# Kernel optimization log

Hardware: AMD Instinct MI355X
Metric: run time of the kernel (lower is better)

The kernel has to match this reference:

```python
import jax, jax.numpy as jnp
import numpy as np

D = 1024; H = 16; HD = 64; L = 8; V = 2048; FF = 4096; WIN = 256
THETA = 10000.0; EPS = 1e-5; LN_EPS = 1e-5; MAXCYC = 16
NM = 16; NR = 72; NT = 12; ME = 64; RE = 64; TE = 32; TPE = 16; DE = 16
B = 2; S = 1024


def _rotate_half(x):
    # torch: stack((-x[...,1::2], x[...,0::2]), -1).flatten(-2)
    x1 = x[..., ::2]
    x2 = x[..., 1::2]
    return jnp.stack((-x2, x1), axis=-1).reshape(x.shape)


def _rmsnorm(x, w):
    return w * (x * jax.lax.rsqrt(jnp.mean(x * x, axis=-1, keepdims=True) + EPS))


def _layernorm(x, g, b):
    mu = jnp.mean(x, axis=-1, keepdims=True)
    var = jnp.mean((x - mu) ** 2, axis=-1, keepdims=True)
    return (x - mu) * jax.lax.rsqrt(var + LN_EPS) * g + b


def setup_inputs() -> dict:
    key = jax.random.key(0)
    ks = iter(jax.random.split(key, 64))
    w = lambda shape: jax.random.normal(next(ks), shape, jnp.float32) * 0.02
    inp = {
        'tokens': jax.random.randint(next(ks), (B, S), 0, V),
        'mood': jax.random.randint(next(ks), (B,), 0, NM),
        'raga': jax.random.randint(next(ks), (B,), 0, NR),
        'taal': jax.random.randint(next(ks), (B,), 0, NT),
        'tempo': jax.random.uniform(next(ks), (B,), jnp.float32),
        'duration': jax.random.uniform(next(ks), (B,), jnp.float32),
        'taal_cycle_len': 8,
        'tok_emb': w((V, D)),
        'mood_emb': w((NM, ME)), 'raga_emb': w((NR, RE)), 'taal_emb': w((NT, TE)),
        'tempo_w': w((TPE, 1)), 'tempo_b': jnp.zeros((TPE,), jnp.float32),
        'dur_w': w((DE, 1)), 'dur_b': jnp.zeros((DE,), jnp.float32),
        'proj_w': w((D, ME + RE + TE + TPE + DE)), 'proj_b': jnp.zeros((D,), jnp.float32),
        'ln_g': jnp.ones((D,), jnp.float32), 'ln_b': jnp.zeros((D,), jnp.float32),
        'cycle_emb': w((MAXCYC, D)), 'strength_emb': w((4, D)),
        'l_anorm': jnp.ones((L, D), jnp.float32), 'l_fnorm': jnp.ones((L, D), jnp.float32),
        'l_q': w((L, D, D)), 'l_k': w((L, D, D)), 'l_v': w((L, D, D)), 'l_o': w((L, D, D)),
        'l_w1': w((L, FF, D)), 'l_w2': w((L, D, FF)), 'l_w3': w((L, FF, D)),
        'final_norm': jnp.ones((D,), jnp.float32),
        'head_w': w((V, D)),
    }
    return inp


def reference(tokens, mood, raga, taal, tempo, duration, taal_cycle_len,
              tok_emb, mood_emb, raga_emb, taal_emb, tempo_w, tempo_b, dur_w, dur_b,
              proj_w, proj_b, ln_g, ln_b, cycle_emb, strength_emb,
              l_anorm, l_fnorm, l_q, l_k, l_v, l_o, l_w1, l_w2, l_w3,
              final_norm, head_w):
    bsz, seq_len = tokens.shape
    # --- ConditioningModule ---
    tp = tempo[:, None] * tempo_w[:, 0][None, :] + tempo_b      # Linear(1, TPE)
    dp = duration[:, None] * dur_w[:, 0][None, :] + dur_b       # Linear(1, DE)
    cond = jnp.concatenate([mood_emb[mood], raga_emb[raga], taal_emb[taal], tp, dp], axis=-1)
    cond = jax.nn.gelu(cond @ proj_w.T + proj_b, approximate=False)
    cond = _layernorm(cond, ln_g, ln_b)                          # [B, D]
    # --- TaalPositionEncoder (taal_cycle_len is static python int) ---
    cyc = min(int(taal_cycle_len), MAXCYC)
    pos_emb = cycle_emb[jnp.arange(seq_len) % cyc]
    strengths = jnp.full((seq_len,), 3, jnp.int32).at[::int(taal_cycle_len)].set(0)
    taal_pos = pos_emb + strength_emb[strengths]                 # [S, D]
    # --- input embedding ---
    x = tok_emb[tokens] + cond[:, None, :] + taal_pos[None]      # [B, S, D]
    # --- RoPE tables (scaling=1.0) ---
    inv_freq = 1.0 / (THETA ** (jnp.arange(0, HD, 2, jnp.float32) / HD))
    freqs = jnp.outer(jnp.arange(seq_len, dtype=jnp.float32), inv_freq)
    emb = jnp.concatenate([freqs, freqs], axis=-1)               # [S, HD]
    cos = jnp.cos(emb)[None, None]
    sin = jnp.sin(emb)[None, None]
    # --- causal sliding-window mask bias ---
    idx = jnp.arange(seq_len)
    allow = (idx[:, None] >= idx[None, :]) & (idx[:, None] - idx[None, :] < WIN)
    bias = jnp.where(allow, 0.0, -jnp.inf).astype(x.dtype)       # [S, S]
    scale = 1.0 / np.sqrt(HD)

    def block(x, p):
        an, fn, qw, kw, vw, ow, w1, w2, w3 = p
        h = _rmsnorm(x, an)
        q = (h @ qw.T).reshape(bsz, seq_len, H, HD).transpose(0, 2, 1, 3)
        k = (h @ kw.T).reshape(bsz, seq_len, H, HD).transpose(0, 2, 1, 3)
        v = (h @ vw.T).reshape(bsz, seq_len, H, HD).transpose(0, 2, 1, 3)
        q = q * cos + _rotate_half(q) * sin
        k = k * cos + _rotate_half(k) * sin
        scores = jnp.einsum('bhqd,bhkd->bhqk', q, k) * scale + bias
        attn = jax.nn.softmax(scores, axis=-1)
        y = jnp.einsum('bhqk,bhkd->bhqd', attn, v)
        y = y.transpose(0, 2, 1, 3).reshape(bsz, seq_len, D)
        x = x + y @ ow.T
        h2 = _rmsnorm(x, fn)
        x = x + (jax.nn.silu(h2 @ w1.T) * (h2 @ w3.T)) @ w2.T
        return x, None

    x, _ = jax.lax.scan(block, x, (l_anorm, l_fnorm, l_q, l_k, l_v, l_o, l_w1, l_w2, l_w3))
    x = _rmsnorm(x, final_norm)
    return x @ head_w.T                                          # [B, S, V] logits
```

## Files before the change

### kernel.cpp

```cpp
#include <hip/hip_runtime.h>
#include <math.h>

#define D_ 1024
#define H_ 16
#define HD_ 64
#define L_ 8
#define V_ 2048
#define FF_ 4096
#define WIN_ 256
#define B_ 2
#define S_ 1024
#define MAXCYC_ 16

typedef __attribute__((ext_vector_type(4))) float f32x4;
typedef __attribute__((ext_vector_type(8))) short s16x8;

__device__ __forceinline__ unsigned short f2bf(float f) {
  union { float f; unsigned int u; } v; v.f = f;
  unsigned int r = v.u + 0x7FFFu + ((v.u >> 16) & 1u);
  return (unsigned short)(r >> 16);
}

__device__ __forceinline__ float wave_sum(float v) {
  #pragma unroll
  for (int m = 1; m < 64; m <<= 1) v += __shfl_xor(v, m, 64);
  return v;
}

__device__ __forceinline__ void gload16(const unsigned short* g, unsigned short* lds) {
  __builtin_amdgcn_global_load_lds(
      (const __attribute__((address_space(1))) void*)g,
      (__attribute__((address_space(3))) void*)lds,
      16, 0, 0);
}

__global__ __launch_bounds__(256) void cvt_kernel(
    const float* __restrict__ src, unsigned short* __restrict__ dst, int n8)
{
  int i = blockIdx.x*256 + threadIdx.x;
  if (i >= n8) return;
  const float4* s = (const float4*)src + (size_t)i*2;
  float4 a = s[0], b = s[1];
  ushort4 lo, hi;
  lo.x = f2bf(a.x); lo.y = f2bf(a.y); lo.z = f2bf(a.z); lo.w = f2bf(a.w);
  hi.x = f2bf(b.x); hi.y = f2bf(b.y); hi.z = f2bf(b.z); hi.w = f2bf(b.w);
  *(ushort4*)(dst + (size_t)i*8)     = lo;
  *(ushort4*)(dst + (size_t)i*8 + 4) = hi;
}

__global__ __launch_bounds__(256) void cond_kernel(
    const int* mood, const int* raga, const int* taal,
    const float* tempo, const float* duration,
    const float* mood_emb, const float* raga_emb, const float* taal_emb,
    const float* tempo_w, const float* tempo_b, const float* dur_w, const float* dur_b,
    const float* proj_w, const float* proj_b, const float* ln_g, const float* ln_b,
    float* cond)
{
  int b = blockIdx.x;
  int t = threadIdx.x;
  __shared__ float feat[192];
  __shared__ float red[4];
  if (t < 64)        feat[t] = mood_emb[mood[b]*64 + t];
  else if (t < 128)  feat[t] = raga_emb[raga[b]*64 + (t-64)];
  else if (t < 160)  feat[t] = taal_emb[taal[b]*32 + (t-128)];
  else if (t < 176)  feat[t] = tempo[b]*tempo_w[t-160] + tempo_b[t-160];
  else if (t < 192)  feat[t] = duration[b]*dur_w[t-176] + dur_b[t-176];
  __syncthreads();
  float g[4];
  #pragma unroll
  for (int r = 0; r < 4; ++r) {
    int j = t + 256*r;
    const float* w = proj_w + (size_t)j*192;
    float acc = proj_b[j];
    for (int f = 0; f < 192; ++f) acc += feat[f]*w[f];
    g[r] = 0.5f * acc * (1.0f + erff(acc * 0.7071067811865475f));
  }
  int lane = t & 63, wv = t >> 6;
  float s1 = g[0]+g[1]+g[2]+g[3];
  s1 = wave_sum(s1);
  if (lane == 0) red[wv] = s1;
  __syncthreads();
  float mu = (red[0]+red[1]+red[2]+red[3]) * (1.0f/1024.0f);
  __syncthreads();
  float vs = 0.f;
  #pragma unroll
  for (int r = 0; r < 4; ++r) { float d = g[r]-mu; vs += d*d; }
  vs = wave_sum(vs);
  if (lane == 0) red[wv] = vs;
  __syncthreads();
  float var = (red[0]+red[1]+red[2]+red[3]) * (1.0f/1024.0f);
  float is = rsqrtf(var + 1e-5f);
  #pragma unroll
  for (int r = 0; r < 4; ++r) {
    int j = t + 256*r;
    cond[(size_t)b*D_ + j] = (g[r]-mu)*is*ln_g[j] + ln_b[j];
  }
}

__global__ __launch_bounds__(256) void embed_kernel(
    const int* tokens, const float* tok_emb, const float* cond,
    const float* cycle_emb, const float* strength_emb, const int* tcl_p, float* x)
{
  int row = blockIdx.x;
  int b = row >> 10, s = row & 1023;
  int tcl = tcl_p[0];
  int cyc = tcl < MAXCYC_ ? tcl : MAXCYC_;
  int pr  = s % cyc;
  int str = (s % tcl == 0) ? 0 : 3;
  int tok = tokens[row];
  int d = threadIdx.x * 4;
  float4 a = *(const float4*)&tok_emb[(size_t)tok*D_ + d];
  float4 c = *(const float4*)&cond[(size_t)b*D_ + d];
  float4 p = *(const float4*)&cycle_emb[(size_t)pr*D_ + d];
  float4 e = *(const float4*)&strength_emb[(size_t)str*D_ + d];
  float4 o; o.x=a.x+c.x+p.x+e.x; o.y=a.y+c.y+p.y+e.y; o.z=a.z+c.z+p.z+e.z; o.w=a.w+c.w+p.w+e.w;
  *(float4*)&x[(size_t)row*D_ + d] = o;
}

__global__ __launch_bounds__(256) void rmsnorm_kernel(
    const float* x, const float* w, unsigned short* out)
{
  int row = blockIdx.x;
  int t = threadIdx.x;
  __shared__ float red[4];
  const float* xr = x + (size_t)row*D_;
  float4 v = *(const float4*)&xr[t*4];
  float ss = v.x*v.x + v.y*v.y + v.z*v.z + v.w*v.w;
  ss = wave_sum(ss);
  int lane = t & 63, wv = t >> 6;
  if (lane == 0) red[wv] = ss;
  __syncthreads();
  float total = red[0]+red[1]+red[2]+red[3];
  float scale = rsqrtf(total * (1.0f/1024.0f) + 1e-5f);
  float4 wv4 = *(const float4*)&w[t*4];
  ushort4 o;
  o.x = f2bf(wv4.x * v.x * scale);
  o.y = f2bf(wv4.y * v.y * scale);
  o.z = f2bf(wv4.z * v.z * scale);
  o.w = f2bf(wv4.w * v.w * scale);
  *(ushort4*)&out[(size_t)row*D_ + t*4] = o;
}

__global__ __launch_bounds__(256) void rope_table_kernel(float* costab, float* sintab)
{
  int i = blockIdx.x*256 + threadIdx.x;
  int s = i >> 6, d = i & 63;
  float inv = powf(10000.0f, -(float)(d & 31) * (1.0f/32.0f));
  float ang = (float)s * inv;
  float sn, cs;
  sincosf(ang, &sn, &cs);
  costab[i] = cs; sintab[i] = sn;
}

__global__ __launch_bounds__(256) void attn_mfma(
    const unsigned short* __restrict__ q, const unsigned short* __restrict__ k,
    const unsigned short* __restrict__ v, unsigned short* __restrict__ y)
{
  __shared__ unsigned short Ks[64*64];
  __shared__ unsigned short VsT[64*72];
  __shared__ unsigned short Ps[4*16*72];

  int qb0 = blockIdx.x * 64;
  int h = blockIdx.y, b = blockIdx.z;
  int t = threadIdx.x, lane = t & 63, wv = t >> 6;
  int c = lane & 15, q4 = lane >> 4;
  unsigned short* Pw = &Ps[wv*16*72];

  s16x8 aq[2];
  {
    const unsigned short* qp =
        q + ((size_t)(b*S_ + qb0 + wv*16 + c)*D_ + h*HD_ + q4*8);
    aq[0] = *(const s16x8*)qp;
    aq[1] = *(const s16x8*)(qp + 32);
  }

  f32x4 o[4];
  #pragma unroll
  for (int j = 0; j < 4; ++j) o[j] = (f32x4){0.f,0.f,0.f,0.f};
  float m[4] = {-1e30f,-1e30f,-1e30f,-1e30f};
  float l[4] = {0.f,0.f,0.f,0.f};

  int skey = t >> 2;
  int scol = (t & 3) * 16;
  int kt0 = qb0 - 256; if (kt0 < 0) kt0 = 0;

  for (int kt = kt0; kt <= qb0; kt += 64) {
    __syncthreads();
    {
      const unsigned short* kp = k + ((size_t)(b*S_ + kt + skey)*D_ + h*HD_ + scol);
      s16x8 k0 = *(const s16x8*)kp;
      s16x8 k1 = *(const s16x8*)(kp + 8);
      int ch0 = scol >> 3;
      *(s16x8*)((char*)Ks + skey*128 + ((ch0 ^ (skey & 7)) << 4)) = k0;
      *(s16x8*)((char*)Ks + skey*128 + (((ch0+1) ^ (skey & 7)) << 4)) = k1;
      const unsigned short* vp = v + ((size_t)(b*S_ + kt + skey)*D_ + h*HD_ + scol);
      s16x8 v0 = *(const s16x8*)vp;
      s16x8 v1 = *(const s16x8*)(vp + 8);
      #pragma unroll
      for (int i = 0; i < 8; ++i) {
        VsT[(scol + i)*72 + skey]     = (unsigned short)v0[i];
        VsT[(scol + 8 + i)*72 + skey] = (unsigned short)v1[i];
      }
    }
    __syncthreads();

    f32x4 sa[4];
    #pragma unroll
    for (int j = 0; j < 4; ++j) sa[j] = (f32x4){0.f,0.f,0.f,0.f};
    #pragma unroll
    for (int ks = 0; ks < 2; ++ks)
      #pragma unroll
      for (int j = 0; j < 4; ++j) {
        int key = j*16 + c;
        s16x8 bk = *(const s16x8*)((const char*)Ks + key*128 +
                                   (((q4 + ks*4) ^ (key & 7)) << 4));
        sa[j] = __builtin_amdgcn_mfma_f32_16x16x32_bf16(aq[ks], bk, sa[j], 0, 0, 0);
      }

    float sv[4][4];
    #pragma unroll
    for (int j = 0; j < 4; ++j) {
      int kg = kt + j*16 + c;
      #pragma unroll
      for (int reg = 0; reg < 4; ++reg) {
        int qg = qb0 + wv*16 + q4*4 + reg;
        bool ok = (qg >= kg) && (qg - kg < WIN_);
        sv[j][reg] = ok ? sa[j][reg]*0.125f : -3e38f;
      }
    }
    #pragma unroll
    for (int reg = 0; reg < 4; ++reg) {
      float mx = fmaxf(fmaxf(sv[0][reg], sv[1][reg]), fmaxf(sv[2][reg], sv[3][reg]));
      #pragma unroll
      for (int msk = 1; msk < 16; msk <<= 1)
        mx = fmaxf(mx, __shfl_xor(mx, msk, 64));
      float nm = fmaxf(m[reg], mx);
      float f = __expf(m[reg] - nm);
      m[reg] = nm;
      l[reg] *= f;
      o[0][reg] *= f; o[1][reg] *= f; o[2][reg] *= f; o[3][reg] *= f;
      float ps = 0.f;
      #pragma unroll
      for (int j = 0; j < 4; ++j) {
        float p = __expf(sv[j][reg] - nm);
        ps += p;
        Pw[(q4*4 + reg)*72 + j*16 + c] = f2bf(p);
      }
      l[reg] += ps;
    }

    #pragma unroll
    for (int ks = 0; ks < 2; ++ks) {
      s16x8 pa = *(const s16x8*)((const char*)Pw + c*144 + (q4 + ks*4)*16);
      #pragma unroll
      for (int j = 0; j < 4; ++j) {
        s16x8 bv = *(const s16x8*)((const char*)VsT + (j*16 + c)*144 + (q4 + ks*4)*16);
        o[j] = __builtin_amdgcn_mfma_f32_16x16x32_bf16(pa, bv, o[j], 0, 0, 0);
      }
    }
  }

  float inv[4];
  #pragma unroll
  for (int reg = 0; reg < 4; ++reg) {
    float ll = l[reg];
    #pragma unroll
    for (int msk = 1; msk < 16; msk <<= 1) ll += __shfl_xor(ll, msk, 64);
    inv[reg] = 1.0f / ll;
  }
  #pragma unroll
  for (int j = 0; j < 4; ++j)
    #pragma unroll
    for (int reg = 0; reg < 4; ++reg)
      Pw[(q4*4 + reg)*72 + j*16 + c] = f2bf(o[j][reg] * inv[reg]);
  int lr = lane >> 2, cc = (lane & 3)*16;
  s16x8 y0 = *(const s16x8*)((const char*)Pw + lr*144 + cc*2);
  s16x8 y1 = *(const s16x8*)((const char*)Pw + lr*144 + cc*2 + 16);
  unsigned short* yp = y + ((size_t)(b*S_ + qb0 + wv*16 + lr)*D_ + h*HD_ + cc);
  *(s16x8*)yp = y0;
  *(s16x8*)(yp + 8) = y1;
}

__global__ __launch_bounds__(256, 2) void gemm_w13(
    const unsigned short* __restrict__ A,
    const unsigned short* __restrict__ W1, const unsigned short* __restrict__ W3,
    unsigned short* __restrict__ T, int K, int lda, int ldw)
{
  __shared__ unsigned short sA[2][128*32];
  __shared__ unsigned short sW1[2][128*32];
  __shared__ unsigned short sW3[2][128*32];
  int tid = threadIdx.x, lane = tid & 63, wave = tid >> 6;
  int wr = (wave >> 1)*64, wc = (wave & 1)*64;
  size_t bm = (size_t)blockIdx.x*128, bn = (size_t)blockIdx.y*128;
  int fr = lane & 15, fk = (lane >> 4)*8, fq = (lane >> 4)*4;
  int rseg = lane >> 2, chunk = (lane & 3)*8;

  f32x4 a1[4][4], a3[4][4];
  #pragma unroll
  for (int i = 0; i < 4; ++i)
    #pragma unroll
    for (int j = 0; j < 4; ++j) {
      a1[i][j] = (f32x4){0.f,0.f,0.f,0.f};
      a3[i][j] = (f32x4){0.f,0.f,0.f,0.f};
    }

  auto stage = [&](int buf, int kt) {
    #pragma unroll
    for (int p = 0; p < 2; ++p) {
      int seg = wave*2 + p;
      int row = seg*16 + rseg;
      gload16(A  + (bm + row)*(size_t)lda + kt + chunk, &sA[buf][seg*512]);
      gload16(W1 + (bn + row)*(size_t)ldw + kt + chunk, &sW1[buf][seg*512]);
      gload16(W3 + (bn + row)*(size_t)ldw + kt + chunk, &sW3[buf][seg*512]);
    }
  };

  stage(0, 0);
  __syncthreads();
  int nt = K >> 5;
  for (int t = 0; t < nt; ++t) {
    int cur = t & 1;
    if (t + 1 < nt) stage(cur ^ 1, (t+1)*32);
    s16x8 af[4], b1[4], b3[4];
    #pragma unroll
    for (int i = 0; i < 4; ++i) {
      af[i] = *(const s16x8*)&sA[cur][(wr + i*16 + fr)*32 + fk];
      b1[i] = *(const s16x8*)&sW1[cur][(wc + i*16 + fr)*32 + fk];
      b3[i] = *(const s16x8*)&sW3[cur][(wc + i*16 + fr)*32 + fk];
    }
    #pragma unroll
    for (int i = 0; i < 4; ++i)
      #pragma unroll
      for (int j = 0; j < 4; ++j) {
        a1[i][j] = __builtin_amdgcn_mfma_f32_16x16x32_bf16(af[i], b1[j], a1[i][j], 0, 0, 0);
        a3[i][j] = __builtin_amdgcn_mfma_f32_16x16x32_bf16(af[i], b3[j], a3[i][j], 0, 0, 0);
      }
    __syncthreads();
  }

  #pragma unroll
  for (int i = 0; i < 4; ++i)
    #pragma unroll
    for (int j = 0; j < 4; ++j) {
      size_t row0 = bm + wr + i*16 + fq;
      size_t col  = bn + wc + j*16 + fr;
      #pragma unroll
      for (int qi = 0; qi < 4; ++qi) {
        float u = a1[i][j][qi];
        float g = a3[i][j][qi];
        float su = u / (1.0f + __expf(-u));
        T[(row0 + qi)*(size_t)FF_ + col] = f2bf(su * g);
      }
    }
}

template<int EPI>
__device__ __forceinline__ void gemm64_core(
    const unsigned short* __restrict__ A, const unsigned short* __restrict__ W,
    float* __restrict__ Cf, unsigned short* __restrict__ Cb,
    int K, int lda, int ldw, int ldc,
    const float* __restrict__ costab, const float* __restrict__ sintab)
{
  __shared__ unsigned short sA[2][128*32];
  __shared__ unsigned short sW[2][64*32];
  int tid = threadIdx.x, lane = tid & 63, wave = tid >> 6;
  int wr = (wave >> 1)*64, wc = (wave & 1)*32;
  size_t bm = (size_t)blockIdx.x*128, bn = (size_t)blockIdx.y*64;
  int fr = lane & 15, fk = (lane >> 4)*8, fq = (lane >> 4)*4;
  int rseg = lane >> 2, chunk = (lane & 3)*8;

  f32x4 acc[4][2];
  #pragma unroll
  for (int i = 0; i < 4; ++i) {
    acc[i][0] = (f32x4){0.f,0.f,0.f,0.f};
    acc[i][1] = (f32x4){0.f,0.f,0.f,0.f};
  }

  auto stage = [&](int buf, int kt) {
    #pragma unroll
    for (int p = 0; p < 2; ++p) {
      int seg = wave*2 + p;
      int row = seg*16 + rseg;
      gload16(A + (bm + row)*(size_t)lda + kt + chunk, &sA[buf][seg*512]);
    }
    int row = wave*16 + rseg;
    gload16(W + (bn + row)*(size_t)ldw + kt + chunk, &sW[buf][wave*512]);
  };

  stage(0, 0);
  __syncthreads();
  int nt = K >> 5;
  for (int t = 0; t < nt; ++t) {
    int cur = t & 1;
    if (t + 1 < nt) stage(cur ^ 1, (t+1)*32);
    s16x8 af[4], bw[2];
    #pragma unroll
    for (int i = 0; i < 4; ++i)
      af[i] = *(const s16x8*)&sA[cur][(wr + i*16 + fr)*32 + fk];
    #pragma unroll
    for (int j = 0; j < 2; ++j)
      bw[j] = *(const s16x8*)&sW[cur][(wc + j*16 + fr)*32 + fk];
    #pragma unroll
    for (int i = 0; i < 4; ++i)
      #pragma unroll
      for (int j = 0; j < 2; ++j)
        acc[i][j] = __builtin_amdgcn_mfma_f32_16x16x32_bf16(af[i], bw[j], acc[i][j], 0, 0, 0);
    __syncthreads();
  }

  #pragma unroll
  for (int i = 0; i < 4; ++i)
    #pragma unroll
    for (int j = 0; j < 2; ++j) {
      size_t row0 = bm + wr + i*16 + fq;
      size_t col  = bn + wc + j*16 + fr;
      #pragma unroll
      for (int qi = 0; qi < 4; ++qi) {
        float val = acc[i][j][qi];
        size_t idx = (row0 + qi)*(size_t)ldc + col;
        if (EPI == 3) {
          float pv = __shfl_xor(val, 1, 64);
          int srow = (int)((row0 + qi) & 1023);
          int d = (int)(col & 63);
          float cs = costab[srow*64 + d];
          float sn = sintab[srow*64 + d];
          Cb[idx] = f2bf(val*cs + ((d & 1) ? pv : -pv)*sn);
        } else if (EPI == 4) {
          Cb[idx] = f2bf(val);
        } else if (EPI == 1) {
          Cf[idx] += val;
        } else {
          Cf[idx] = val;
        }
      }
    }
}

template<int EPI>
__global__ __launch_bounds__(256) void gemm64(
    const unsigned short* __restrict__ A, const unsigned short* __restrict__ W,
    float* __restrict__ Cf, int K, int lda, int ldw, int ldc)
{
  gemm64_core<EPI>(A, W, Cf, nullptr, K, lda, ldw, ldc, nullptr, nullptr);
}

__global__ __launch_bounds__(256) void gemm_qkv64(
    const unsigned short* __restrict__ A,
    const unsigned short* __restrict__ Wq, const unsigned short* __restrict__ Wk,
    const unsigned short* __restrict__ Wv,
    unsigned short* __restrict__ Cq, unsigned short* __restrict__ Ck,
    unsigned short* __restrict__ Cv,
    const float* __restrict__ costab, const float* __restrict__ sintab)
{
  if (blockIdx.z == 0)
    gemm64_core<3>(A, Wq, nullptr, Cq, D_, D_, D_, D_, costab, sintab);
  else if (blockIdx.z == 1)
    gemm64_core<3>(A, Wk, nullptr, Ck, D_, D_, D_, D_, costab, sintab);
  else
    gemm64_core<4>(A, Wv, nullptr, Cv, D_, D_, D_, D_, nullptr, nullptr);
}

extern "C" void kernel_launch(void* const* d_in, const int* in_sizes, int n_in,
                              void* d_out, int out_size, void* d_ws, size_t ws_size,
                              hipStream_t stream)
{
  const int*   tokens    = (const int*)d_in[0];
  const int*   mood      = (const int*)d_in[1];
  const int*   raga      = (const int*)d_in[2];
  const int*   taal      = (const int*)d_in[3];
  const float* tempo     = (const float*)d_in[4];
  const float* duration  = (const float*)d_in[5];
  const int*   tcl       = (const int*)d_in[6];
  const float* tok_emb   = (const float*)d_in[7];
  const float* mood_emb  = (const float*)d_in[8];
  const float* raga_emb  = (const float*)d_in[9];
  const float* taal_emb  = (const float*)d_in[10];
  const float* tempo_w   = (const float*)d_in[11];
  const float* tempo_b   = (const float*)d_in[12];
  const float* dur_w     = (const float*)d_in[13];
  const float* dur_b     = (const float*)d_in[14];
  const float* proj_w    = (const float*)d_in[15];
  const float* proj_b    = (const float*)d_in[16];
  const float* ln_g      = (const float*)d_in[17];
  const float* ln_b      = (const float*)d_in[18];
  const float* cycle_emb = (const float*)d_in[19];
  const float* strength_e= (const float*)d_in[20];
  const float* l_anorm   = (const float*)d_in[21];
  const float* l_fnorm   = (const float*)d_in[22];
  const float* l_q       = (const float*)d_in[23];
  const float* l_k       = (const float*)d_in[24];
  const float* l_v       = (const float*)d_in[25];
  const float* l_o       = (const float*)d_in[26];
  const float* l_w1      = (const float*)d_in[27];
  const float* l_w2      = (const float*)d_in[28];
  const float* l_w3      = (const float*)d_in[29];
  const float* final_norm= (const float*)d_in[30];
  const float* head_w    = (const float*)d_in[31];

  size_t off = 0;
  char* wsb = (char*)d_ws;
  auto alloc = [&](size_t bytes) -> char* {
    char* p = wsb + off;
    off += (bytes + 255) & ~(size_t)255;
    return p;
  };
  float*          condb  = (float*)alloc((size_t)B_*D_*4);
  float*          costab = (float*)alloc((size_t)S_*HD_*4);
  float*          sintab = (float*)alloc((size_t)S_*HD_*4);
  float*          x      = (float*)alloc((size_t)B_*S_*D_*4);
  unsigned short* hbuf   = (unsigned short*)alloc((size_t)B_*S_*D_*2);
  unsigned short* qb     = (unsigned short*)alloc((size_t)B_*S_*D_*2);
  unsigned short* kb     = (unsigned short*)alloc((size_t)B_*S_*D_*2);
  unsigned short* vb     = (unsigned short*)alloc((size_t)B_*S_*D_*2);
  unsigned short* yb     = (unsigned short*)alloc((size_t)B_*S_*D_*2);
  unsigned short* tb     = (unsigned short*)alloc((size_t)B_*S_*FF_*2);

  const size_t N_QKVO = (size_t)L_*D_*D_;
  const size_t N_FF   = (size_t)L_*FF_*D_;
  const size_t N_HEAD = (size_t)V_*D_;
  unsigned short* wbf = (unsigned short*)alloc((4*N_QKVO + 3*N_FF + N_HEAD)*2);
  unsigned short* bq = wbf;
  unsigned short* bk = wbf + N_QKVO;
  unsigned short* bv = wbf + 2*N_QKVO;
  unsigned short* bo = wbf + 3*N_QKVO;
  unsigned short* b1 = wbf + 4*N_QKVO;
  unsigned short* b2 = wbf + 4*N_QKVO + N_FF;
  unsigned short* b3 = wbf + 4*N_QKVO + 2*N_FF;
  unsigned short* bh = wbf + 4*N_QKVO + 3*N_FF;

  rope_table_kernel<<<(S_*HD_)/256, 256, 0, stream>>>(costab, sintab);
  cond_kernel<<<B_, 256, 0, stream>>>(mood, raga, taal, tempo, duration,
      mood_emb, raga_emb, taal_emb, tempo_w, tempo_b, dur_w, dur_b,
      proj_w, proj_b, ln_g, ln_b, condb);
  embed_kernel<<<B_*S_, 256, 0, stream>>>(tokens, tok_emb, condb, cycle_emb,
      strength_e, tcl, x);

  cvt_kernel<<<(int)(N_QKVO/8/256), 256, 0, stream>>>(l_q,  bq, (int)(N_QKVO/8));
  cvt_kernel<<<(int)(N_QKVO/8/256), 256, 0, stream>>>(l_k,  bk, (int)(N_QKVO/8));
  cvt_kernel<<<(int)(N_QKVO/8/256), 256, 0, stream>>>(l_v,  bv, (int)(N_QKVO/8));
  cvt_kernel<<<(int)(N_QKVO/8/256), 256, 0, stream>>>(l_o,  bo, (int)(N_QKVO/8));
  cvt_kernel<<<(int)(N_FF/8/256),   256, 0, stream>>>(l_w1, b1, (int)(N_FF/8));
  cvt_kernel<<<(int)(N_FF/8/256),   256, 0, stream>>>(l_w2, b2, (int)(N_FF/8));
  cvt_kernel<<<(int)(N_FF/8/256),   256, 0, stream>>>(l_w3, b3, (int)(N_FF/8));
  cvt_kernel<<<(int)(N_HEAD/8/256), 256, 0, stream>>>(head_w, bh, (int)(N_HEAD/8));

  const int rows = B_*S_;
  for (int l = 0; l < L_; ++l) {
    size_t dd = (size_t)l*D_*D_;
    size_t fd = (size_t)l*FF_*D_;
    rmsnorm_kernel<<<rows, 256, 0, stream>>>(x, l_anorm + (size_t)l*D_, hbuf);
    gemm_qkv64<<<dim3(rows/128, D_/64, 3), 256, 0, stream>>>(
        hbuf, bq + dd, bk + dd, bv + dd, qb, kb, vb, costab, sintab);
    attn_mfma<<<dim3(S_/64, H_, B_), 256, 0, stream>>>(qb, kb, vb, yb);
    gemm64<1><<<dim3(rows/128, D_/64), 256, 0, stream>>>(
        yb, bo + dd, x, D_, D_, D_, D_);
    rmsnorm_kernel<<<rows, 256, 0, stream>>>(x, l_fnorm + (size_t)l*D_, hbuf);
    gemm_w13<<<dim3(rows/128, FF_/128), 256, 0, stream>>>(
        hbuf, b1 + fd, b3 + fd, tb, D_, D_, D_);
    gemm64<1><<<dim3(rows/128, D_/64), 256, 0, stream>>>(
        tb, b2 + fd, x, FF_, FF_, FF_, D_);
  }
  rmsnorm_kernel<<<rows, 256, 0, stream>>>(x, final_norm, hbuf);
  gemm64<0><<<dim3(rows/128, V_/64), 256, 0, stream>>>(
      hbuf, bh, (float*)d_out, D_, D_, D_, V_);
}
```

Before: 1.898 ms.

## Split-K the O/W2 projections, fuse residual add into RMSNorm, swizzle LDS tiles

Result: faster. 1.782 ms (-6.1%).

```diff
diff --git a/kernel.cpp b/kernel.cpp
--- a/kernel.cpp
+++ b/kernel.cpp
@@ -141,6 +141,37 @@
   *(ushort4*)&out[(size_t)row*D_ + t*4] = o;
 }
 
+__global__ __launch_bounds__(256) void resid_rmsnorm_kernel(
+    float* __restrict__ x, const float* __restrict__ part, int nparts,
+    const float* __restrict__ w, unsigned short* __restrict__ out)
+{
+  int row = blockIdx.x;
+  int t = threadIdx.x;
+  __shared__ float red[4];
+  size_t base = (size_t)row*D_ + t*4;
+  const size_t pstride = (size_t)B_*S_*D_;
+  float4 v = *(const float4*)&x[base];
+  for (int p = 0; p < nparts; ++p) {
+    float4 a = *(const float4*)&part[p*pstride + base];
+    v.x += a.x; v.y += a.y; v.z += a.z; v.w += a.w;
+  }
+  *(float4*)&x[base] = v;
+  float ss = v.x*v.x + v.y*v.y + v.z*v.z + v.w*v.w;
+  ss = wave_sum(ss);
+  int lane = t & 63, wv = t >> 6;
+  if (lane == 0) red[wv] = ss;
+  __syncthreads();
+  float total = red[0]+red[1]+red[2]+red[3];
+  float scale = rsqrtf(total * (1.0f/1024.0f) + 1e-5f);
+  float4 wv4 = *(const float4*)&w[t*4];
+  ushort4 o;
+  o.x = f2bf(wv4.x * v.x * scale);
+  o.y = f2bf(wv4.y * v.y * scale);
+  o.z = f2bf(wv4.z * v.z * scale);
+  o.w = f2bf(wv4.w * v.w * scale);
+  *(ushort4*)&out[(size_t)row*D_ + t*4] = o;
+}
+
 __global__ __launch_bounds__(256) void rope_table_kernel(float* costab, float* sintab)
 {
   int i = blockIdx.x*256 + threadIdx.x;
@@ -292,8 +323,9 @@
   int tid = threadIdx.x, lane = tid & 63, wave = tid >> 6;
   int wr = (wave >> 1)*64, wc = (wave & 1)*64;
   size_t bm = (size_t)blockIdx.x*128, bn = (size_t)blockIdx.y*128;
-  int fr = lane & 15, fk = (lane >> 4)*8, fq = (lane >> 4)*4;
-  int rseg = lane >> 2, chunk = (lane & 3)*8;
+  int fr = lane & 15, q4 = lane >> 4, fq = q4*4;
+  int lrow = lane >> 2;
+  int gcol = ((lane & 3) ^ (lrow & 3)) * 8;
 
   f32x4 a1[4][4], a3[4][4];
   #pragma unroll
@@ -308,10 +340,10 @@
     #pragma unroll
     for (int p = 0; p < 2; ++p) {
       int seg = wave*2 + p;
-      int row = seg*16 + rseg;
-      gload16(A  + (bm + row)*(size_t)lda + kt + chunk, &sA[buf][seg*512]);
-      gload16(W1 + (bn + row)*(size_t)ldw + kt + chunk, &sW1[buf][seg*512]);
-      gload16(W3 + (bn + row)*(size_t)ldw + kt + chunk, &sW3[buf][seg*512]);
+      size_t row = (size_t)(seg*16 + lrow);
+      gload16(A  + (bm + row)*(size_t)lda + kt + gcol, &sA[buf][seg*512]);
+      gload16(W1 + (bn + row)*(size_t)ldw + kt + gcol, &sW1[buf][seg*512]);
+      gload16(W3 + (bn + row)*(size_t)ldw + kt + gcol, &sW3[buf][seg*512]);
     }
   };
 
@@ -324,9 +356,10 @@
     s16x8 af[4], b1[4], b3[4];
     #pragma unroll
     for (int i = 0; i < 4; ++i) {
-      af[i] = *(const s16x8*)&sA[cur][(wr + i*16 + fr)*32 + fk];
-      b1[i] = *(const s16x8*)&sW1[cur][(wc + i*16 + fr)*32 + fk];
-      b3[i] = *(const s16x8*)&sW3[cur][(wc + i*16 + fr)*32 + fk];
+      int ra = wr + i*16 + fr, rb = wc + i*16 + fr;
+      af[i] = *(const s16x8*)((const char*)&sA[cur][0]  + ra*64 + ((q4 ^ (ra & 3)) << 4));
+      b1[i] = *(const s16x8*)((const char*)&sW1[cur][0] + rb*64 + ((q4 ^ (rb & 3)) << 4));
+      b3[i] = *(const s16x8*)((const char*)&sW3[cur][0] + rb*64 + ((q4 ^ (rb & 3)) << 4));
     }
     #pragma unroll
     for (int i = 0; i < 4; ++i)
@@ -358,16 +391,17 @@
 __device__ __forceinline__ void gemm64_core(
     const unsigned short* __restrict__ A, const unsigned short* __restrict__ W,
     float* __restrict__ Cf, unsigned short* __restrict__ Cb,
-    int K, int lda, int ldw, int ldc,
+    int kbase, int Kslice, int lda, int ldw, int ldc,
     const float* __restrict__ costab, const float* __restrict__ sintab)
 {
-  __shared__ unsigned short sA[2][128*32];
-  __shared__ unsigned short sW[2][64*32];
+  __shared__ unsigned short sA[2][128*64];
+  __shared__ unsigned short sW[2][64*64];
   int tid = threadIdx.x, lane = tid & 63, wave = tid >> 6;
   int wr = (wave >> 1)*64, wc = (wave & 1)*32;
   size_t bm = (size_t)blockIdx.x*128, bn = (size_t)blockIdx.y*64;
-  int fr = lane & 15, fk = (lane >> 4)*8, fq = (lane >> 4)*4;
-  int rseg = lane >> 2, chunk = (lane & 3)*8;
+  int fr = lane & 15, q4 = lane >> 4, fq = q4*4;
+  int lrow = lane >> 3;
+  int gcol = ((lane & 7) ^ lrow) * 8;
 
   f32x4 acc[4][2];
   #pragma unroll
@@ -378,33 +412,44 @@
 
   auto stage = [&](int buf, int kt) {
     #pragma unroll
+    for (int p = 0; p < 4; ++p) {
+      int seg = wave*4 + p;
+      gload16(A + (bm + seg*8 + lrow)*(size_t)lda + kt + gcol, &sA[buf][seg*512]);
+    }
+    #pragma unroll
     for (int p = 0; p < 2; ++p) {
       int seg = wave*2 + p;
-      int row = seg*16 + rseg;
-      gload16(A + (bm + row)*(size_t)lda + kt + chunk, &sA[buf][seg*512]);
-    }
-    int row = wave*16 + rseg;
-    gload16(W + (bn + row)*(size_t)ldw + kt + chunk, &sW[buf][wave*512]);
+      gload16(W + (bn + seg*8 + lrow)*(size_t)ldw + kt + gcol, &sW[buf][seg*512]);
+    }
   };
 
-  stage(0, 0);
-  __syncthreads();
-  int nt = K >> 5;
+  stage(0, kbase);
+  __syncthreads();
+  int nt = Kslice >> 6;
   for (int t = 0; t < nt; ++t) {
     int cur = t & 1;
-    if (t + 1 < nt) stage(cur ^ 1, (t+1)*32);
-    s16x8 af[4], bw[2];
-    #pragma unroll
-    for (int i = 0; i < 4; ++i)
-      af[i] = *(const s16x8*)&sA[cur][(wr + i*16 + fr)*32 + fk];
-    #pragma unroll
-    for (int j = 0; j < 2; ++j)
-      bw[j] = *(const s16x8*)&sW[cur][(wc + j*16 + fr)*32 + fk];
-    #pragma unroll
-    for (int i = 0; i < 4; ++i)
-      #pragma unroll
-      for (int j = 0; j < 2; ++j)
-        acc[i][j] = __builtin_amdgcn_mfma_f32_16x16x32_bf16(af[i], bw[j], acc[i][j], 0, 0, 0);
+    if (t + 1 < nt) stage(cur ^ 1, kbase + (t+1)*64);
+    #pragma unroll
+    for (int ks = 0; ks < 2; ++ks) {
+      s16x8 af[4], bw[2];
+      #pragma unroll
+      for (int i = 0; i < 4; ++i) {
+        int r = wr + i*16 + fr;
+        af[i] = *(const s16x8*)((const char*)&sA[cur][0] + r*128 +
+                                ((((ks<<2) + q4) ^ (r & 7)) << 4));
+      }
+      #pragma unroll
+      for (int j = 0; j < 2; ++j) {
+        int r = wc + j*16 + fr;
+        bw[j] = *(const s16x8*)((const char*)&sW[cur][0] + r*128 +
+                                ((((ks<<2) + q4) ^ (r & 7)) << 4));
+      }
+      #pragma unroll
+      for (int i = 0; i < 4; ++i)
+        #pragma unroll
+        for (int j = 0; j < 2; ++j)
+          acc[i][j] = __builtin_amdgcn_mfma_f32_16x16x32_bf16(af[i], bw[j], acc[i][j], 0, 0, 0);
+    }
     __syncthreads();
   }
 
@@ -427,8 +472,6 @@
           Cb[idx] = f2bf(val*cs + ((d & 1) ? pv : -pv)*sn);
         } else if (EPI == 4) {
           Cb[idx] = f2bf(val);
-        } else if (EPI == 1) {
-          Cf[idx] += val;
         } else {
           Cf[idx] = val;
         }
@@ -437,14 +480,23 @@
 }
 
 template<int EPI>
-__global__ __launch_bounds__(256) void gemm64(
+__global__ __launch_bounds__(256, 3) void gemm64(
     const unsigned short* __restrict__ A, const unsigned short* __restrict__ W,
     float* __restrict__ Cf, int K, int lda, int ldw, int ldc)
 {
-  gemm64_core<EPI>(A, W, Cf, nullptr, K, lda, ldw, ldc, nullptr, nullptr);
-}
-
-__global__ __launch_bounds__(256) void gemm_qkv64(
+  gemm64_core<EPI>(A, W, Cf, nullptr, 0, K, lda, ldw, ldc, nullptr, nullptr);
+}
+
+__global__ __launch_bounds__(256, 3) void gemm64_ksplit(
+    const unsigned short* __restrict__ A, const unsigned short* __restrict__ W,
+    float* __restrict__ P, int Kslice, int lda, int ldw, int ldc)
+{
+  float* out = P + (size_t)blockIdx.z * (size_t)B_ * S_ * ldc;
+  gemm64_core<0>(A, W, out, nullptr, blockIdx.z*Kslice, Kslice, lda, ldw, ldc,
+                 nullptr, nullptr);
+}
+
+__global__ __launch_bounds__(256, 3) void gemm_qkv64(
     const unsigned short* __restrict__ A,
     const unsigned short* __restrict__ Wq, const unsigned short* __restrict__ Wk,
     const unsigned short* __restrict__ Wv,
@@ -453,11 +505,11 @@
     const float* __restrict__ costab, const float* __restrict__ sintab)
 {
   if (blockIdx.z == 0)
-    gemm64_core<3>(A, Wq, nullptr, Cq, D_, D_, D_, D_, costab, sintab);
+    gemm64_core<3>(A, Wq, nullptr, Cq, 0, D_, D_, D_, D_, costab, sintab);
   else if (blockIdx.z == 1)
-    gemm64_core<3>(A, Wk, nullptr, Ck, D_, D_, D_, D_, costab, sintab);
+    gemm64_core<3>(A, Wk, nullptr, Ck, 0, D_, D_, D_, D_, costab, sintab);
   else
-    gemm64_core<4>(A, Wv, nullptr, Cv, D_, D_, D_, D_, nullptr, nullptr);
+    gemm64_core<4>(A, Wv, nullptr, Cv, 0, D_, D_, D_, D_, nullptr, nullptr);
 }
 
 extern "C" void kernel_launch(void* const* d_in, const int* in_sizes, int n_in,
@@ -514,6 +566,7 @@
   unsigned short* vb     = (unsigned short*)alloc((size_t)B_*S_*D_*2);
   unsigned short* yb     = (unsigned short*)alloc((size_t)B_*S_*D_*2);
   unsigned short* tb     = (unsigned short*)alloc((size_t)B_*S_*FF_*2);
+  float*          pbuf   = (float*)alloc((size_t)4*B_*S_*D_*4);
 
   const size_t N_QKVO = (size_t)L_*D_*D_;
   const size_t N_FF   = (size_t)L_*FF_*D_;
@@ -545,22 +598,24 @@
   cvt_kernel<<<(int)(N_HEAD/8/256), 256, 0, stream>>>(head_w, bh, (int)(N_HEAD/8));
 
   const int rows = B_*S_;
+  rmsnorm_kernel<<<rows, 256, 0, stream>>>(x, l_anorm, hbuf);
   for (int l = 0; l < L_; ++l) {
     size_t dd = (size_t)l*D_*D_;
     size_t fd = (size_t)l*FF_*D_;
-    rmsnorm_kernel<<<rows, 256, 0, stream>>>(x, l_anorm + (size_t)l*D_, hbuf);
     gemm_qkv64<<<dim3(rows/128, D_/64, 3), 256, 0, stream>>>(
         hbuf, bq + dd, bk + dd, bv + dd, qb, kb, vb, costab, sintab);
     attn_mfma<<<dim3(S_/64, H_, B_), 256, 0, stream>>>(qb, kb, vb, yb);
-    gemm64<1><<<dim3(rows/128, D_/64), 256, 0, stream>>>(
-        yb, bo + dd, x, D_, D_, D_, D_);
-    rmsnorm_kernel<<<rows, 256, 0, stream>>>(x, l_fnorm + (size_t)l*D_, hbuf);
+    gemm64_ksplit<<<dim3(rows/128, D_/64, 2), 256, 0, stream>>>(
+        yb, bo + dd, pbuf, 512, D_, D_, D_);
+    resid_rmsnorm_kernel<<<rows, 256, 0, stream>>>(
+        x, pbuf, 2, l_fnorm + (size_t)l*D_, hbuf);
     gemm_w13<<<dim3(rows/128, FF_/128), 256, 0, stream>>>(
         hbuf, b1 + fd, b3 + fd, tb, D_, D_, D_);
-    gemm64<1><<<dim3(rows/128, D_/64), 256, 0, stream>>>(
-        tb, b2 + fd, x, FF_, FF_, FF_, D_);
-  }
-  rmsnorm_kernel<<<rows, 256, 0, stream>>>(x, final_norm, hbuf);
+    gemm64_ksplit<<<dim3(rows/128, D_/64, 4), 256, 0, stream>>>(
+        tb, b2 + fd, pbuf, 1024, FF_, FF_, D_);
+    const float* nextw = (l+1 < L_) ? (l_anorm + (size_t)(l+1)*D_) : final_norm;
+    resid_rmsnorm_kernel<<<rows, 256, 0, stream>>>(x, pbuf, 4, nextw, hbuf);
+  }
   gemm64<0><<<dim3(rows/128, V_/64), 256, 0, stream>>>(
       hbuf, bh, (float*)d_out, D_, D_, D_, V_);
 }
```
